# Performance work log

Hardware: AMD Instinct MI355X
Metric: run time of the kernel (lower is better)

The kernel has to match this reference:

```python
import jax, jax.numpy as jnp
import numpy as np

N = 50000          # nodes
E = 400000         # edges (before self loops)
F_IN = 128         # NUM_FEATURES
HID = 32           # hidden_dim
H = 12             # heads
HC = H * HID       # concat dim = 384
CLASSES = 40       # NUM_CLASSES
NEG_SLOPE = 0.2    # PyG GATv2 default


def setup_inputs() -> dict:
    key = jax.random.key(0)
    ks = jax.random.split(key, 16)

    def p(k, shape, fan_in):
        return (jax.random.normal(k, shape, jnp.float32) / np.sqrt(fan_in)).astype(jnp.float32)

    return {
        "x": jax.random.normal(ks[0], (N, F_IN), jnp.float32),
        "edge_index": jax.random.randint(ks[1], (2, E), 0, N, jnp.int32),
        # GATv2 layer 1 (share_weights=False)
        "Wl1": p(ks[2], (F_IN, HC), F_IN),
        "Wr1": p(ks[3], (F_IN, HC), F_IN),
        "a1": p(ks[4], (H, HID), HID),
        "b1": jnp.zeros((HC,), jnp.float32),
        # GATv2 layer 2
        "Wl2": p(ks[5], (HC, HC), HC),
        "Wr2": p(ks[6], (HC, HC), HC),
        "a2": p(ks[7], (H, HID), HID),
        "b2": jnp.zeros((HC,), jnp.float32),
        # MLP head
        "W3": p(ks[8], (HC, HID), HC),
        "b3": jnp.zeros((HID,), jnp.float32),
        "W4": p(ks[9], (HID, CLASSES), HID),
        "b4": jnp.zeros((CLASSES,), jnp.float32),
    }


def _gatv2(x, Wl, Wr, att, bias, src, dst):
    # source/target linear projections, per-head
    xl = (x @ Wl).reshape(-1, H, HID)   # [N,H,C] (message features)
    xr = (x @ Wr).reshape(-1, H, HID)   # [N,H,C]
    # per-edge attention logits: a^T LeakyReLU(xl_src + xr_dst)
    e = jax.nn.leaky_relu(xl[src] + xr[dst], NEG_SLOPE)   # [E',H,C]
    logit = jnp.einsum('ehc,hc->eh', e, att)              # [E',H]
    # segment softmax over incoming edges per dst node (self loops guarantee nonempty)
    m = jax.ops.segment_max(logit, dst, num_segments=N)   # [N,H]
    ex = jnp.exp(logit - m[dst])
    denom = jax.ops.segment_sum(ex, dst, num_segments=N)  # [N,H]
    alpha = ex / denom[dst]                                # [E',H]
    # weighted scatter-add of source messages
    out = jax.ops.segment_sum(xl[src] * alpha[:, :, None], dst, num_segments=N)
    return out.reshape(-1, HC) + bias


def reference(x, edge_index, Wl1, Wr1, a1, b1, Wl2, Wr2, a2, b2, W3, b3, W4, b4):
    # add_self_loops=True (PyG default)
    loops = jnp.arange(N, dtype=edge_index.dtype)
    src = jnp.concatenate([edge_index[0], loops])
    dst = jnp.concatenate([edge_index[1], loops])
    # dropout p=0.6 is identity in eval mode
    h = _gatv2(x, Wl1, Wr1, a1, b1, src, dst)
    h = jax.nn.elu(h)
    h = _gatv2(h, Wl2, Wr2, a2, b2, src, dst)
    h = jax.nn.elu(h)
    h = jax.nn.elu(h @ W3 + b3)
    h = h @ W4 + b4
    return jax.nn.log_softmax(h, axis=1)
```

## Files before the change

### kernel.cpp

```cpp
#include <hip/hip_runtime.h>
#include <hip/hip_bf16.h>
#include <math.h>

#define N_NODES 50000
#define E_EDGES 400000
#define EN_TOT  (E_EDGES + N_NODES)
#define F_IN    128
#define HC      384
#define CLASSES 40
#define LOG2E   1.44269504088896f

typedef short short8 __attribute__((ext_vector_type(8)));
typedef float floatx4 __attribute__((ext_vector_type(4)));
typedef float floatx2 __attribute__((ext_vector_type(2)));
typedef unsigned int uint;

struct u3 { uint x, y, z; };

__device__ __forceinline__ float bf2f(unsigned short u) {
  union { unsigned int i; float f; } x; x.i = ((unsigned int)u) << 16; return x.f;
}
__device__ __forceinline__ unsigned short f2bf(float f) {
  union { float f; unsigned int i; } x; x.f = f;
  unsigned int r = x.i + 0x7fffu + ((x.i >> 16) & 1u);
  return (unsigned short)(r >> 16);
}
__device__ __forceinline__ float fin(float v) {
  return (fabsf(v) < 1e30f) ? v : 0.f;
}
__device__ __forceinline__ float rdw(const void* p, int idx, int fp32) {
  return fp32 ? ((const float*)p)[idx] : bf2f(((const unsigned short*)p)[idx]);
}

#if __has_builtin(__builtin_amdgcn_exp2f)
#define EXP2F(x) __builtin_amdgcn_exp2f(x)
#else
#define EXP2F(x) exp2f(x)
#endif

#if __has_builtin(__builtin_amdgcn_update_dpp)
#define DPP_ADD(w, ctrl) \
  (w += __int_as_float(__builtin_amdgcn_update_dpp(0, __float_as_int(w), ctrl, 0xf, 0xf, true)))
#define REDUCE16(w) do { DPP_ADD(w, 0xB1); DPP_ADD(w, 0x4E); DPP_ADD(w, 0x141); DPP_ADD(w, 0x140); } while (0)
#define DPP_MAXF(w, ctrl) do { float _t = __int_as_float(__builtin_amdgcn_update_dpp(0, \
    __float_as_int(w), ctrl, 0xf, 0xf, true)); w = fmaxf(w, _t); } while (0)
#define RED16MAX(w) do { DPP_MAXF(w, 0xB1); DPP_MAXF(w, 0x4E); DPP_MAXF(w, 0x141); DPP_MAXF(w, 0x140); } while (0)
#else
#define REDUCE16(w) do { w += __shfl_xor(w, 1); w += __shfl_xor(w, 2); \
                         w += __shfl_xor(w, 4); w += __shfl_xor(w, 8); } while (0)
#define RED16MAX(w) do { w = fmaxf(w, __shfl_xor(w, 1)); w = fmaxf(w, __shfl_xor(w, 2)); \
                         w = fmaxf(w, __shfl_xor(w, 4)); w = fmaxf(w, __shfl_xor(w, 8)); } while (0)
#endif


__global__ void k_sentinel(float* out, int n) {
  int i = blockIdx.x * 256 + threadIdx.x;
  if (i < n) out[i] = 111.0f;
}

__global__ void k_detect(const unsigned short* __restrict__ x, int* __restrict__ flag) {
  int L = threadIdx.x;
  int sane = 0;
#pragma unroll
  for (int t = 0; t < 4; ++t) {
    unsigned short u = x[(size_t)(L * 4 + t) * 2];
    unsigned int mag = u & 0x7FFFu;
    unsigned int e   = (u >> 7) & 0xFFu;
    if (mag == 0u || (e >= 96u && e <= 159u)) sane++;
  }
  sane += __shfl_xor(sane, 1);
  sane += __shfl_xor(sane, 2);
  sane += __shfl_xor(sane, 4);
  sane += __shfl_xor(sane, 8);
  sane += __shfl_xor(sane, 16);
  sane += __shfl_xor(sane, 32);
  if (L == 0) flag[0] = (sane < 179) ? 1 : 0;
}

__global__ void k_count(const int* __restrict__ ei, int* __restrict__ counts) {
  int e = blockIdx.x * 256 + threadIdx.x;
  if (e >= EN_TOT) return;
  int dst = (e < E_EDGES) ? ei[E_EDGES + e] : (e - E_EDGES);
  if ((unsigned)dst < N_NODES) atomicAdd(&counts[dst], 1);
}

__global__ void k_scan1(const int* __restrict__ counts, int* __restrict__ row_start,
                        int* __restrict__ bsum) {
  int b = blockIdx.x, tid = threadIdx.x;
  int i = b * 1024 + tid;
  int v = (i < N_NODES) ? counts[i] : 0;
  int lane = tid & 63, w = tid >> 6;
  int x = v;
#pragma unroll
  for (int d = 1; d < 64; d <<= 1) { int t = __shfl_up(x, d); if (lane >= d) x += t; }
  __shared__ int wsum[16];
  if (lane == 63) wsum[w] = x;
  __syncthreads();
  if (w == 0) {
    int y = (lane < 16) ? wsum[lane] : 0;
#pragma unroll
    for (int d = 1; d < 16; d <<= 1) { int t = __shfl_up(y, d); if (lane >= d) y += t; }
    if (lane < 16) wsum[lane] = y;
  }
  __syncthreads();
  if (w > 0) x += wsum[w - 1];
  if (i < N_NODES) row_start[i + 1] = x;
  if (tid == 1023) bsum[b] = x;
}

__global__ void k_scan23(int* __restrict__ row_start, const int* __restrict__ bsum, int nb) {
  int b = blockIdx.x, tid = threadIdx.x;
  __shared__ int sadd;
  if (tid < 64) {
    int lane = tid;
    int x = (lane < nb) ? bsum[lane] : 0;
#pragma unroll
    for (int d = 1; d < 64; d <<= 1) { int t = __shfl_up(x, d); if (lane >= d) x += t; }
    int pre = __shfl(x, (b > 0) ? (b - 1) : 0);
    if (tid == 0) sadd = (b > 0) ? pre : 0;
  }
  __syncthreads();
  int add = sadd;
  int i = b * 1024 + tid;
  if (i < N_NODES) row_start[i + 1] += add;
  if (i == 0) row_start[0] = 0;
}

__global__ void k_fill(const int* __restrict__ ei, const int* __restrict__ row_start,
                       int* __restrict__ cursor, int* __restrict__ csr_off) {
  int e = blockIdx.x * 256 + threadIdx.x;
  if (e >= EN_TOT) return;
  int src, dst;
  if (e < E_EDGES) { src = ei[e]; dst = ei[E_EDGES + e]; }
  else             { src = dst = e - E_EDGES; }
  if ((unsigned)dst >= N_NODES) return;
  int sv = ((unsigned)src < N_NODES) ? src : 0;
  int pos = atomicAdd(&cursor[dst], 1);
  int slot = row_start[dst] + pos;
  if ((unsigned)slot < EN_TOT) csr_off[slot] = sv * 768;
}

#define PK_J1 (F_IN * HC)
#define PK_J2 (2 * PK_J1)
#define PK_J3 (PK_J2 + HC * HC)
#define PK_J4 (PK_J3 + HC * HC)
#define PK_J5 (PK_J4 + HC * 32)
#define PK_J6 (PK_J5 + 32 * 48)
#define PK_EX 3144
#define PK_TOT (PK_J6 + PK_EX)
__global__ void k_pack_all(const void* __restrict__ Wl1, const void* __restrict__ Wr1,
                           const void* __restrict__ Wl2, const void* __restrict__ Wr2,
                           const void* __restrict__ W3, const void* __restrict__ W4,
                           const void* __restrict__ a1_, const void* __restrict__ a2_,
                           const void* __restrict__ b1_, const void* __restrict__ b2_,
                           const void* __restrict__ b3_, const void* __restrict__ b4_,
                           unsigned short* __restrict__ BpL1, unsigned short* __restrict__ BpR1,
                           unsigned short* __restrict__ BpL2, unsigned short* __restrict__ BpR2,
                           unsigned short* __restrict__ Bp3, unsigned short* __restrict__ Bp4,
                           float* __restrict__ attp1, float* __restrict__ attp2,
                           float* __restrict__ biasp1, float* __restrict__ biasp2,
                           float* __restrict__ b3p, float* __restrict__ b4p,
                           const int* __restrict__ flagp) {
  int gid = blockIdx.x * 256 + threadIdx.x;
  if (gid >= PK_TOT) return;
  int fp32 = flagp[0];
  if (gid >= PK_J6) {
    int i = gid - PK_J6;
    if (i < 3072) {
      int seg = i / 768, r = i % 768;
      int L = r / 6, q = r % 6, k = q >> 1, b = q & 1;
      int c = 2 * L + 128 * k + b;
      if (seg == 0)      attp1[r]  = fin(rdw(a1_, c, fp32)) * LOG2E;
      else if (seg == 1) attp2[r]  = fin(rdw(a2_, c, fp32)) * LOG2E;
      else if (seg == 2) biasp1[r] = fin(rdw(b1_, c, fp32));
      else               biasp2[r] = fin(rdw(b2_, c, fp32));
    } else if (i < 3104) b3p[i - 3072] = fin(rdw(b3_, i - 3072, fp32));
    else                 b4p[i - 3104] = fin(rdw(b4_, i - 3104, fp32));
    return;
  }
  const void* src; unsigned short* dst; int NT, NCOL, idx;
  if (gid < PK_J2)      { NT = 24; NCOL = 384; if (gid < PK_J1) { src = Wl1; dst = BpL1; idx = gid; }
                                               else             { src = Wr1; dst = BpR1; idx = gid - PK_J1; } }
  else if (gid < PK_J4) { NT = 24; NCOL = 384; if (gid < PK_J3) { src = Wl2; dst = BpL2; idx = gid - PK_J2; }
                                               else             { src = Wr2; dst = BpR2; idx = gid - PK_J3; } }
  else if (gid < PK_J5) { NT = 2;  NCOL = 32;  src = W3; dst = Bp3; idx = gid - PK_J4; }
  else                  { NT = 3;  NCOL = 40;  src = W4; dst = Bp4; idx = gid - PK_J5; }
  int j  = idx & 7;
  int L  = (idx >> 3) & 63;
  int t  = idx >> 9;
  int nt = t % NT;
  int kt = t / NT;
  int k  = kt * 32 + ((L >> 4) * 8) + j;
  int n  = nt * 16 + (L & 15);
  float v = (n < NCOL) ? rdw(src, k * NCOL + n, fp32) : 0.f;
  dst[idx] = f2bf(fin(v));
}

#define LOADB(dst, kt) do { _Pragma("unroll") for (int n = 0; n < 6; ++n) \
    dst[n] = ((const short8*)Bp)[((size_t)((kt) * 24 + nt0 + n)) * 64 + lane]; } while (0)
#define DOMFMA(bf, kt) do { \
    short8 af[2]; \
    _Pragma("unroll") for (int mf = 0; mf < 2; ++mf) { \
      int row = mf * 16 + rsel; \
      int col = (kt) * 64 + kk16 * 16; \
      af[mf] = *(const short8*)(smem + row * RS + (col ^ ((row & 7) << 4))); } \
    _Pragma("unroll") for (int n = 0; n < 6; ++n) \
      _Pragma("unroll") for (int mf = 0; mf < 2; ++mf) \
        acc[mf][n] = __builtin_amdgcn_mfma_f32_16x16x32_bf16(af[mf], bf[n], acc[mf][n], 0, 0, 0); } while (0)

template<int NK, int AF>
__global__ __launch_bounds__(256, 4) void k_gemm2(const void* __restrict__ A_,
                       const unsigned short* __restrict__ BpL,
                       const unsigned short* __restrict__ BpR,
                       unsigned short* __restrict__ CL, unsigned short* __restrict__ CR,
                       const int* __restrict__ flagp) {
  constexpr int RS  = NK * 64;
  constexpr int NST = NK / 2;
  __shared__ __align__(16) char smem[32 * 776];
  int which = blockIdx.x & 1;
  int bt    = blockIdx.x >> 1;
  const unsigned short* Bp = which ? BpR : BpL;
  unsigned short* C        = which ? CR  : CL;
  int fp32 = AF ? flagp[0] : 0;
  int tid  = threadIdx.x;
  int wave = tid >> 6, lane = tid & 63;
  int m0   = bt * 32;

  {
    uint4 v[NST];
#pragma unroll
    for (int i = 0; i < NST; ++i) {
      int o   = (i * 256 + tid) * 16;
      int row = o / RS;
      int rem = o - row * RS;
      int rg  = m0 + row; if (rg >= N_NODES) rg = N_NODES - 1;
      if (AF && fp32) {
        const float* p = (const float*)((const char*)A_ + ((size_t)rg * RS + rem) * 2);
        floatx4 f0 = *(const floatx4*)p;
        floatx4 f1 = *(const floatx4*)(p + 4);
        short8 o8;
#pragma unroll
        for (int j = 0; j < 4; ++j) { o8[j] = (short)f2bf(f0[j]); o8[4 + j] = (short)f2bf(f1[j]); }
        v[i] = *(uint4*)&o8;
      } else {
        v[i] = *(const uint4*)((const char*)A_ + (size_t)rg * RS + rem);
      }
    }
#pragma unroll
    for (int i = 0; i < NST; ++i) {
      int o   = (i * 256 + tid) * 16;
      int row = o / RS;
      int rem = o - row * RS;
      *(uint4*)(smem + row * RS + (rem ^ ((row & 7) << 4))) = v[i];
    }
  }

  int nt0  = wave * 6;
  int kk16 = (lane >> 4);
  int rsel = lane & 15;
  floatx4 acc[2][6];
#pragma unroll
  for (int mf = 0; mf < 2; ++mf)
#pragma unroll
    for (int n = 0; n < 6; ++n) acc[mf][n] = (floatx4){0.f, 0.f, 0.f, 0.f};

  short8 b0[6], b1[6], b2[6];
  LOADB(b0, 0);
  LOADB(b1, 1);
  __syncthreads();

#pragma unroll
  for (int kt = 0; kt < NK; ++kt) {
    if (kt + 2 < NK) {
      if (((kt + 2) % 3) == 0)      LOADB(b0, kt + 2);
      else if (((kt + 2) % 3) == 1) LOADB(b1, kt + 2);
      else                          LOADB(b2, kt + 2);
    }
    if ((kt % 3) == 0)      DOMFMA(b0, kt);
    else if ((kt % 3) == 1) DOMFMA(b1, kt);
    else                    DOMFMA(b2, kt);
  }

  __syncthreads();
  int qr = lane >> 4, ccol = lane & 15;
#pragma unroll
  for (int n = 0; n < 6; ++n) {
    int c    = (nt0 + n) * 16 + ccol;
    int soff = ((c & 127) >> 1) * 12 + (c >> 7) * 4 + (c & 1) * 2;
#pragma unroll
    for (int mf = 0; mf < 2; ++mf)
#pragma unroll
      for (int r = 0; r < 4; ++r) {
        int row = mf * 16 + qr * 4 + r;
        *(unsigned short*)(smem + row * 776 + soff) = f2bf(fin(acc[mf][n][r]));
      }
  }
  __syncthreads();
#pragma unroll
  for (int j = 0; j < 8; ++j) {
    int row = wave * 8 + j;
    int rg  = m0 + row;
    if (rg < N_NODES) {
      u3 val = *(const u3*)(smem + row * 776 + lane * 12);
      *(u3*)((char*)C + (size_t)rg * 768 + lane * 12) = val;
    }
  }
}

#define EBODY(q) do { \
    uint _qa[3] = {(q).x, (q).y, (q).z}; \
    _Pragma("unroll") \
    for (int k = 0; k < 3; ++k) { \
      floatx2 sv; \
      sv.x = __uint_as_float(_qa[k] << 16); \
      sv.y = __uint_as_float(_qa[k] & 0xffff0000u); \
      floatx2 t = sv + r2[k]; \
      t = __builtin_elementwise_max(t, t * 0.2f); \
      floatx2 dw = t * a2[k]; \
      float w = dw.x + dw.y; \
      REDUCE16(w); \
      w = fminf(fmaxf(w, -126.f), 126.f); \
      float p = EXP2F(w); \
      l[k] += p; \
      floatx2 pv = {p, p}; \
      acc[k] += pv * sv; \
    } } while (0)

__global__ void k_edge(const unsigned short* __restrict__ XL, const unsigned short* __restrict__ XR,
                       const int* __restrict__ row_start, const int* __restrict__ csr_off,
                       const float* __restrict__ attp, const float* __restrict__ biasp,
                       unsigned short* __restrict__ H) {
  int v = blockIdx.x;
  int L = threadIdx.x;
  int Lo = L * 12;
  floatx2 r2[3], a2[3];
  u3 rv3 = *(const u3*)((const char*)XR + (size_t)v * 768 + Lo);
  uint rr[3] = {rv3.x, rv3.y, rv3.z};
  const floatx2* ap = (const floatx2*)(attp + L * 6);
#pragma unroll
  for (int k = 0; k < 3; ++k) {
    r2[k].x = __uint_as_float(rr[k] << 16);
    r2[k].y = __uint_as_float(rr[k] & 0xffff0000u);
    a2[k] = ap[k];
  }
  float l[3] = {0.f, 0.f, 0.f};
  floatx2 acc[3];
#pragma unroll
  for (int k = 0; k < 3; ++k) acc[k] = (floatx2){0.f, 0.f};
  int beg = row_start[v], end = row_start[v + 1];
  if (beg < 0) beg = 0;
  if (end > EN_TOT) end = EN_TOT;
  const char* XLb = (const char*)XL;
  const unsigned OMAX = (N_NODES - 1) * 768u;
  for (int base = beg; base < end; base += 64) {
    int nE = end - base; if (nE > 64) nE = 64;
    int last = nE - 1;
    int offv = (base + L < end) ? csr_off[base + L] : 0;
#define RLD(i) ({ int _i = (i) > last ? last : (i); \
                  int _s = __builtin_amdgcn_readlane(offv, _i); \
                  if ((unsigned)_s > OMAX) _s = 0; \
                  *(const u3*)(XLb + (unsigned)_s + Lo); })
    u3 q0 = RLD(0), q1 = RLD(1), q2 = RLD(2), q3 = RLD(3);
    u3 q4 = RLD(4), q5 = RLD(5), q6 = RLD(6), q7 = RLD(7);
    int j = 0;
    for (; j + 8 <= nE; j += 8) {
      u3 n0 = RLD(j + 8),  n1 = RLD(j + 9),  n2 = RLD(j + 10), n3 = RLD(j + 11);
      u3 n4 = RLD(j + 12), n5 = RLD(j + 13), n6 = RLD(j + 14), n7 = RLD(j + 15);
      EBODY(q0); EBODY(q1); EBODY(q2); EBODY(q3);
      EBODY(q4); EBODY(q5); EBODY(q6); EBODY(q7);
      q0 = n0; q1 = n1; q2 = n2; q3 = n3;
      q4 = n4; q5 = n5; q6 = n6; q7 = n7;
    }
    if (j < nE)     EBODY(q0);
    if (j + 1 < nE) EBODY(q1);
    if (j + 2 < nE) EBODY(q2);
    if (j + 3 < nE) EBODY(q3);
    if (j + 4 < nE) EBODY(q4);
    if (j + 5 < nE) EBODY(q5);
    if (j + 6 < nE) EBODY(q6);
#undef RLD
  }
  const floatx2* bp = (const floatx2*)(biasp + L * 6);
  uint* hr = (uint*)(H + (size_t)v * HC);
#pragma unroll
  for (int k = 0; k < 3; ++k) {
    floatx2 bb = bp[k];
    float inv = 1.f / fmaxf(l[k], 1e-30f);
    float o0 = acc[k].x * inv + bb.x;
    float o1 = acc[k].y * inv + bb.y;
    o0 = o0 > 0.f ? o0 : EXP2F(o0 * LOG2E) - 1.f;
    o1 = o1 > 0.f ? o1 : EXP2F(o1 * LOG2E) - 1.f;
    hr[L + 64 * k] = (uint)f2bf(fin(o0)) | ((uint)f2bf(fin(o1)) << 16);
  }
}

__global__ void k_mlp(const unsigned short* __restrict__ H2,
                      const unsigned short* __restrict__ Bp3,
                      const unsigned short* __restrict__ Bp4,
                      const float* __restrict__ b3p, const float* __restrict__ b4p,
                      float* __restrict__ out) {
  __shared__ float hs[16][33];
  int lane = threadIdx.x;
  int m0   = blockIdx.x * 16;
  int row  = m0 + (lane & 15);
  int kk   = (lane >> 4) * 8;
  floatx4 acc[2];
  acc[0] = (floatx4){0.f, 0.f, 0.f, 0.f};
  acc[1] = (floatx4){0.f, 0.f, 0.f, 0.f};
#pragma unroll
  for (int kt = 0; kt < 12; ++kt) {
    short8 af = *(const short8*)(H2 + (size_t)row * HC + kt * 32 + kk);
    const short8* bp = (const short8*)Bp3 + (size_t)kt * 2 * 64 + lane;
    acc[0] = __builtin_amdgcn_mfma_f32_16x16x32_bf16(af, bp[0],  acc[0], 0, 0, 0);
    acc[1] = __builtin_amdgcn_mfma_f32_16x16x32_bf16(af, bp[64], acc[1], 0, 0, 0);
  }
  int qr = lane >> 4, cc = lane & 15;
#pragma unroll
  for (int nt = 0; nt < 2; ++nt)
#pragma unroll
    for (int r = 0; r < 4; ++r) {
      int col = nt * 16 + cc;
      float s = acc[nt][r] + b3p[col];
      s = s > 0.f ? s : EXP2F(s * LOG2E) - 1.f;
      hs[qr * 4 + r][col] = fin(s);
    }
  __syncthreads();
  short8 a2f;
#pragma unroll
  for (int j = 0; j < 8; ++j) a2f[j] = (short)f2bf(hs[lane & 15][kk + j]);
  floatx4 lg[3];
#pragma unroll
  for (int nt = 0; nt < 3; ++nt) {
    floatx4 z = (floatx4){0.f, 0.f, 0.f, 0.f};
    lg[nt] = __builtin_amdgcn_mfma_f32_16x16x32_bf16(a2f, ((const short8*)Bp4)[nt * 64 + lane], z, 0, 0, 0);
  }
  float bv[3];
#pragma unroll
  for (int nt = 0; nt < 3; ++nt) {
    int c = nt * 16 + cc;
    bv[nt] = (c < CLASSES) ? b4p[c] : 0.f;
  }
#pragma unroll
  for (int r = 0; r < 4; ++r) {
    float v0 = lg[0][r] + bv[0];
    float v1 = lg[1][r] + bv[1];
    float v2 = (cc < 8) ? (lg[2][r] + bv[2]) : -1e30f;
    float mx = fmaxf(fmaxf(v0, v1), v2);
    RED16MAX(mx);
    float sm = __expf(v0 - mx) + __expf(v1 - mx) + ((cc < 8) ? __expf(v2 - mx) : 0.f);
    sm = (sm == sm) ? sm : 1.f;
    REDUCE16(sm);
    float ls = mx + logf(sm);
    float* op = out + (size_t)(m0 + qr * 4 + r) * CLASSES;
    op[cc]      = fin(v0 - ls);
    op[16 + cc] = fin(v1 - ls);
    if (cc < 8) op[32 + cc] = fin(v2 - ls);
  }
}

extern "C" void kernel_launch(void* const* d_in, const int* in_sizes, int n_in,
                              void* d_out, int out_size, void* d_ws, size_t ws_size,
                              hipStream_t stream) {
  const void* x   = d_in[0];
  const int* ei   = (const int*)d_in[1];
  const void* Wl1 = d_in[2];
  const void* Wr1 = d_in[3];
  const void* a1  = d_in[4];
  const void* b1  = d_in[5];
  const void* Wl2 = d_in[6];
  const void* Wr2 = d_in[7];
  const void* a2  = d_in[8];
  const void* b2  = d_in[9];
  const void* W3  = d_in[10];
  const void* b3  = d_in[11];
  const void* W4  = d_in[12];
  const void* b4  = d_in[13];
  float* out = (float*)d_out;

  char* ws = (char*)d_ws;
  size_t off = 0;
  auto alloc = [&](size_t bytes) { size_t o = off; off += (bytes + 255) & ~(size_t)255; return o; };
  int* flag       = (int*)(ws + alloc(256));
  int* row_start  = (int*)(ws + alloc((size_t)(N_NODES + 1) * 4));
  int* counts     = (int*)(ws + alloc((size_t)2 * N_NODES * 4));
  int* cursor     = counts + N_NODES;
  int* bsum       = (int*)(ws + alloc(64 * 4));
  int* csr_off    = (int*)(ws + alloc((size_t)EN_TOT * 4));
  unsigned short* BpL1 = (unsigned short*)(ws + alloc((size_t)F_IN * HC * 2));
  unsigned short* BpR1 = (unsigned short*)(ws + alloc((size_t)F_IN * HC * 2));
  unsigned short* BpL2 = (unsigned short*)(ws + alloc((size_t)HC * HC * 2));
  unsigned short* BpR2 = (unsigned short*)(ws + alloc((size_t)HC * HC * 2));
  unsigned short* Bp3  = (unsigned short*)(ws + alloc((size_t)HC * 32 * 2));
  unsigned short* Bp4  = (unsigned short*)(ws + alloc((size_t)32 * 48 * 2));
  float* attp1  = (float*)(ws + alloc(768 * 4));
  float* attp2  = (float*)(ws + alloc(768 * 4));
  float* biasp1 = (float*)(ws + alloc(768 * 4));
  float* biasp2 = (float*)(ws + alloc(768 * 4));
  float* b3p    = (float*)(ws + alloc(32 * 4));
  float* b4p    = (float*)(ws + alloc(40 * 4));
  unsigned short* B0   = (unsigned short*)(ws + alloc((size_t)N_NODES * HC * 2));
  unsigned short* B1   = (unsigned short*)(ws + alloc((size_t)N_NODES * HC * 2));
  unsigned short* B2   = (unsigned short*)(ws + alloc((size_t)N_NODES * HC * 2));
  (void)in_sizes; (void)n_in;

  if (ws_size < off) {
    k_sentinel<<<(out_size + 255) / 256, 256, 0, stream>>>(out, out_size);
    return;
  }

  const int SCAN_BLOCKS = (N_NODES + 1023) / 1024;
  const int GEMM_BLOCKS = 2 * ((N_NODES + 31) / 32);

  hipMemsetAsync(counts, 0, (size_t)2 * N_NODES * 4, stream);
  k_detect<<<1, 64, 0, stream>>>((const unsigned short*)x, flag);
  k_count<<<(EN_TOT + 255) / 256, 256, 0, stream>>>(ei, counts);
  k_scan1<<<SCAN_BLOCKS, 1024, 0, stream>>>(counts, row_start, bsum);
  k_scan23<<<SCAN_BLOCKS, 1024, 0, stream>>>(row_start, bsum, SCAN_BLOCKS);
  k_fill<<<(EN_TOT + 255) / 256, 256, 0, stream>>>(ei, row_start, cursor, csr_off);

  k_pack_all<<<(PK_TOT + 255) / 256, 256, 0, stream>>>(Wl1, Wr1, Wl2, Wr2, W3, W4,
                                                       a1, a2, b1, b2, b3, b4,
                                                       BpL1, BpR1, BpL2, BpR2, Bp3, Bp4,
                                                       attp1, attp2, biasp1, biasp2, b3p, b4p, flag);

  k_gemm2<4, 1><<<GEMM_BLOCKS, 256, 0, stream>>>(x, BpL1, BpR1, B0, B1, flag);
  k_edge<<<N_NODES, 64, 0, stream>>>(B0, B1, row_start, csr_off, attp1, biasp1, B1);

  k_gemm2<12, 0><<<GEMM_BLOCKS, 256, 0, stream>>>(B1, BpL2, BpR2, B2, B0, flag);
  k_edge<<<N_NODES, 64, 0, stream>>>(B2, B0, row_start, csr_off, attp2, biasp2, B1);

  k_mlp<<<N_NODES / 16, 64, 0, stream>>>(B1, Bp3, Bp4, b3p, b4p, out);
}
```

Measured before the change: 366.6 us.

## Pack four nodes per edge block, shrink prefetch depth, fuse zeroing into detect

The edge aggregation kernel now runs four 64-lane waves per 256-thread block, one node per wave, instead of one-wave blocks. Its software prefetch ring drops from 8 to 4 rows to lower register pressure and raise occupancy. The memset and the detect kernel are merged into one kernel that zeroes counts and cursor, removing a launch. The risk is less memory-level parallelism per wave from the shallower prefetch.

```diff
diff --git a/kernel.cpp b/kernel.cpp
--- a/kernel.cpp
+++ b/kernel.cpp
@@ -58,23 +58,28 @@
   if (i < n) out[i] = 111.0f;
 }
 
-__global__ void k_detect(const unsigned short* __restrict__ x, int* __restrict__ flag) {
-  int L = threadIdx.x;
-  int sane = 0;
-#pragma unroll
-  for (int t = 0; t < 4; ++t) {
-    unsigned short u = x[(size_t)(L * 4 + t) * 2];
-    unsigned int mag = u & 0x7FFFu;
-    unsigned int e   = (u >> 7) & 0xFFu;
-    if (mag == 0u || (e >= 96u && e <= 159u)) sane++;
-  }
-  sane += __shfl_xor(sane, 1);
-  sane += __shfl_xor(sane, 2);
-  sane += __shfl_xor(sane, 4);
-  sane += __shfl_xor(sane, 8);
-  sane += __shfl_xor(sane, 16);
-  sane += __shfl_xor(sane, 32);
-  if (L == 0) flag[0] = (sane < 179) ? 1 : 0;
+__global__ void k_detect_zero(const unsigned short* __restrict__ x, int* __restrict__ flag,
+                              int* __restrict__ counts, int* __restrict__ cursor) {
+  int i = blockIdx.x * 256 + threadIdx.x;
+  if (i < N_NODES) { counts[i] = 0; cursor[i] = 0; }
+  if (blockIdx.x == 0 && threadIdx.x < 64) {
+    int L = threadIdx.x;
+    int sane = 0;
+#pragma unroll
+    for (int t = 0; t < 4; ++t) {
+      unsigned short u = x[(size_t)(L * 4 + t) * 2];
+      unsigned int mag = u & 0x7FFFu;
+      unsigned int e   = (u >> 7) & 0xFFu;
+      if (mag == 0u || (e >= 96u && e <= 159u)) sane++;
+    }
+    sane += __shfl_xor(sane, 1);
+    sane += __shfl_xor(sane, 2);
+    sane += __shfl_xor(sane, 4);
+    sane += __shfl_xor(sane, 8);
+    sane += __shfl_xor(sane, 16);
+    sane += __shfl_xor(sane, 32);
+    if (L == 0) flag[0] = (sane < 179) ? 1 : 0;
+  }
 }
 
 __global__ void k_count(const int* __restrict__ ei, int* __restrict__ counts) {
@@ -326,12 +331,13 @@
       acc[k] += pv * sv; \
     } } while (0)
 
-__global__ void k_edge(const unsigned short* __restrict__ XL, const unsigned short* __restrict__ XR,
+__global__ __launch_bounds__(256) void k_edge(const unsigned short* __restrict__ XL,
+                       const unsigned short* __restrict__ XR,
                        const int* __restrict__ row_start, const int* __restrict__ csr_off,
                        const float* __restrict__ attp, const float* __restrict__ biasp,
                        unsigned short* __restrict__ H) {
-  int v = blockIdx.x;
-  int L = threadIdx.x;
+  int v = blockIdx.x * 4 + (threadIdx.x >> 6);
+  int L = threadIdx.x & 63;
   int Lo = L * 12;
   floatx2 r2[3], a2[3];
   u3 rv3 = *(const u3*)((const char*)XR + (size_t)v * 768 + Lo);
@@ -361,23 +367,15 @@
                   if ((unsigned)_s > OMAX) _s = 0; \
                   *(const u3*)(XLb + (unsigned)_s + Lo); })
     u3 q0 = RLD(0), q1 = RLD(1), q2 = RLD(2), q3 = RLD(3);
-    u3 q4 = RLD(4), q5 = RLD(5), q6 = RLD(6), q7 = RLD(7);
     int j = 0;
-    for (; j + 8 <= nE; j += 8) {
-      u3 n0 = RLD(j + 8),  n1 = RLD(j + 9),  n2 = RLD(j + 10), n3 = RLD(j + 11);
-      u3 n4 = RLD(j + 12), n5 = RLD(j + 13), n6 = RLD(j + 14), n7 = RLD(j + 15);
+    for (; j + 4 <= nE; j += 4) {
+      u3 n0 = RLD(j + 4), n1 = RLD(j + 5), n2 = RLD(j + 6), n3 = RLD(j + 7);
       EBODY(q0); EBODY(q1); EBODY(q2); EBODY(q3);
-      EBODY(q4); EBODY(q5); EBODY(q6); EBODY(q7);
       q0 = n0; q1 = n1; q2 = n2; q3 = n3;
-      q4 = n4; q5 = n5; q6 = n6; q7 = n7;
     }
     if (j < nE)     EBODY(q0);
     if (j + 1 < nE) EBODY(q1);
     if (j + 2 < nE) EBODY(q2);
-    if (j + 3 < nE) EBODY(q3);
-    if (j + 4 < nE) EBODY(q4);
-    if (j + 5 < nE) EBODY(q5);
-    if (j + 6 < nE) EBODY(q6);
 #undef RLD
   }
   const floatx2* bp = (const floatx2*)(biasp + L * 6);
@@ -482,8 +480,8 @@
   auto alloc = [&](size_t bytes) { size_t o = off; off += (bytes + 255) & ~(size_t)255; return o; };
   int* flag       = (int*)(ws + alloc(256));
   int* row_start  = (int*)(ws + alloc((size_t)(N_NODES + 1) * 4));
-  int* counts     = (int*)(ws + alloc((size_t)2 * N_NODES * 4));
-  int* cursor     = counts + N_NODES;
+  int* counts     = (int*)(ws + alloc((size_t)N_NODES * 4));
+  int* cursor     = (int*)(ws + alloc((size_t)N_NODES * 4));
   int* bsum       = (int*)(ws + alloc(64 * 4));
   int* csr_off    = (int*)(ws + alloc((size_t)EN_TOT * 4));
   unsigned short* BpL1 = (unsigned short*)(ws + alloc((size_t)F_IN * HC * 2));
@@ -511,8 +509,7 @@
   const int SCAN_BLOCKS = (N_NODES + 1023) / 1024;
   const int GEMM_BLOCKS = 2 * ((N_NODES + 31) / 32);
 
-  hipMemsetAsync(counts, 0, (size_t)2 * N_NODES * 4, stream);
-  k_detect<<<1, 64, 0, stream>>>((const unsigned short*)x, flag);
+  k_detect_zero<<<(N_NODES + 255) / 256, 256, 0, stream>>>((const unsigned short*)x, flag, counts, cursor);
   k_count<<<(EN_TOT + 255) / 256, 256, 0, stream>>>(ei, counts);
   k_scan1<<<SCAN_BLOCKS, 1024, 0, stream>>>(counts, row_start, bsum);
   k_scan23<<<SCAN_BLOCKS, 1024, 0, stream>>>(row_start, bsum, SCAN_BLOCKS);
@@ -524,10 +521,10 @@
                                                        attp1, attp2, biasp1, biasp2, b3p, b4p, flag);
 
   k_gemm2<4, 1><<<GEMM_BLOCKS, 256, 0, stream>>>(x, BpL1, BpR1, B0, B1, flag);
-  k_edge<<<N_NODES, 64, 0, stream>>>(B0, B1, row_start, csr_off, attp1, biasp1, B1);
+  k_edge<<<N_NODES / 4, 256, 0, stream>>>(B0, B1, row_start, csr_off, attp1, biasp1, B1);
 
   k_gemm2<12, 0><<<GEMM_BLOCKS, 256, 0, stream>>>(B1, BpL2, BpR2, B2, B0, flag);
-  k_edge<<<N_NODES, 64, 0, stream>>>(B2, B0, row_start, csr_off, attp2, biasp2, B1);
+  k_edge<<<N_NODES / 4, 256, 0, stream>>>(B2, B0, row_start, csr_off, attp2, biasp2, B1);
 
   k_mlp<<<N_NODES / 16, 64, 0, stream>>>(B1, Bp3, Bp4, b3p, b4p, out);
 }
```

After: 354.5 us. -3.3%, faster.
